# Kernel optimization log

Hardware: AMD Instinct MI355X
Metric: run time of the kernel (lower is better)

Reference implementation:

```python
import jax, jax.numpy as jnp
import numpy as np

EMBED_DIM = 1024
NUM_HEADS = 16
HEAD_DIM = EMBED_DIM // NUM_HEADS


def setup_inputs() -> dict:
    key = jax.random.key(0)
    ks = jax.random.split(key, 9)
    B, S, D = 2, 2048, EMBED_DIM
    scale = 1.0 / np.sqrt(D)
    x = jax.random.normal(ks[0], (B, S, D), dtype=jnp.float32)
    # Linear params (torch nn.Linear: y = x @ W.T + b); store W as [out, in]
    Wq = jax.random.normal(ks[1], (D, D), dtype=jnp.float32) * scale
    bq = jnp.zeros((D,), dtype=jnp.float32)
    Wk = jax.random.normal(ks[2], (D, D), dtype=jnp.float32) * scale
    bk = jnp.zeros((D,), dtype=jnp.float32)
    Wv = jax.random.normal(ks[3], (D, D), dtype=jnp.float32) * scale
    bv = jnp.zeros((D,), dtype=jnp.float32)
    Wo = jax.random.normal(ks[4], (D, D), dtype=jnp.float32) * scale
    bo = jnp.zeros((D,), dtype=jnp.float32)
    return {"x": x, "Wq": Wq, "bq": bq, "Wk": Wk, "bk": bk,
            "Wv": Wv, "bv": bv, "Wo": Wo, "bo": bo}


def reference(x, Wq, bq, Wk, bk, Wv, bv, Wo, bo):
    B, S, D = x.shape
    H, Hd = NUM_HEADS, HEAD_DIM
    scaling = Hd ** -0.5
    # projections (torch Linear: x @ W.T + b)
    q = (x @ Wq.T + bq).reshape(B, S, H, Hd).transpose(0, 2, 1, 3)  # [B,H,S,Hd]
    k = (x @ Wk.T + bk).reshape(B, S, H, Hd).transpose(0, 2, 1, 3)
    v = (x @ Wv.T + bv).reshape(B, S, H, Hd).transpose(0, 2, 1, 3)
    # full score matrix, as in the original (no flash tiling)
    scores = jnp.einsum('bhqd,bhkd->bhqk', q, k) * scaling  # [B,H,S,S]
    attn = jax.nn.softmax(scores, axis=-1)
    # dropout is identity in eval mode
    out = jnp.einsum('bhqk,bhkd->bhqd', attn, v)  # [B,H,S,Hd]
    out = out.transpose(0, 2, 1, 3).reshape(B, S, D)
    return out @ Wo.T + bo
```

## Files before the change

### kernel.cpp

```cpp
#include <hip/hip_runtime.h>
#include <stdint.h>

typedef unsigned short u16;
typedef short short8 __attribute__((ext_vector_type(8)));
typedef float f32x4 __attribute__((ext_vector_type(4)));
typedef float f32x16 __attribute__((ext_vector_type(16)));
typedef float f32x2 __attribute__((ext_vector_type(2)));

__device__ __forceinline__ u16 f2bf_fast(float f) {
  union { float f; uint32_t u; } x;
  x.f = f;
  return (u16)((x.u + 0x8000u) >> 16);
}

__device__ __forceinline__ uint32_t pack2bf(float lo, float hi) {
  union { float f; uint32_t u; } a, b;
  a.f = lo; b.f = hi;
  return __builtin_amdgcn_perm(b.u + 0x8000u, a.u + 0x8000u, 0x07060302u);
}

__device__ __forceinline__ float bf2f(uint32_t u) {
  union { uint32_t u; float f; } x;
  x.u = u << 16;
  return x.f;
}

__device__ __forceinline__ uint32_t cvtpk(float lo, float hi) {
  uint32_t r;
  asm("v_cvt_pk_bf16_f32 %0, %1, %2" : "=v"(r) : "v"(lo), "v"(hi));
  return r;
}

__device__ __forceinline__ void permswap(uint32_t& a, uint32_t& b) {
  asm("v_permlane32_swap_b32 %0, %1" : "+v"(a), "+v"(b));
}

__device__ __forceinline__ void gload_lds16(const void* g, void* l) {
  __builtin_amdgcn_global_load_lds(
      (const __attribute__((address_space(1))) void*)g,
      (__attribute__((address_space(3))) void*)l, 16, 0, 0);
}

__device__ __forceinline__ f32x4 mfma16(short8 a, short8 b, f32x4 c) {
  return __builtin_amdgcn_mfma_f32_16x16x32_bf16(a, b, c, 0, 0, 0);
}

__device__ __forceinline__ f32x16 mfma32(short8 a, short8 b, f32x16 c) {
  return __builtin_amdgcn_mfma_f32_32x32x16_bf16(a, b, c, 0, 0, 0);
}

#define QSCALE 0.18033688011112042f

__global__ void pack_all(const float* __restrict__ x, const float* __restrict__ wq,
                         const float* __restrict__ wk, const float* __restrict__ wv,
                         const float* __restrict__ wo, u16* __restrict__ xp,
                         u16* __restrict__ wp) {
  const int gi = blockIdx.x * 256 + threadIdx.x;
  const int lane = gi & 63;
  const int kc = (gi >> 6) & 31;
  const int rt = gi >> 11;
  const int col = kc * 32 + (lane >> 4) * 8;
  const float* src;
  int row;
  if (rt < 256) {
    src = x;
    row = rt * 16 + (lane & 15);
  } else {
    const int wti = rt - 256;
    const int widx = wti >> 6;
    src = (widx == 0) ? wq : (widx == 1) ? wk : (widx == 2) ? wv : wo;
    row = (wti & 63) * 16 + (lane & 15);
  }
  const float4* p = (const float4*)(src + (size_t)row * 1024 + col);
  const float4 v0 = p[0], v1 = p[1];
  uint4 o;
  o.x = pack2bf(v0.x, v0.y);
  o.y = pack2bf(v0.z, v0.w);
  o.z = pack2bf(v1.x, v1.y);
  o.w = pack2bf(v1.z, v1.w);
  u16* dst = (rt < 256) ? xp : wp;
  const int og = (rt < 256) ? gi : gi - 524288;
  ((uint4*)dst)[og] = o;
}

__global__ __launch_bounds__(256, 3) void proj_qkv(
    const u16* __restrict__ xp, const u16* __restrict__ wp,
    const float* __restrict__ bq, const float* __restrict__ bk,
    const float* __restrict__ bv, u16* __restrict__ qw, u16* __restrict__ kw,
    u16* __restrict__ vw) {
  __shared__ __align__(16) u16 As[8192];
  __shared__ __align__(16) u16 Bs[8192];
  const int tid = threadIdx.x, lane = tid & 63, w = tid >> 6;
  const int quad = lane >> 4, l15 = lane & 15;

  const int bid = blockIdx.x;
  const int work = (bid & 7) * 96 + (bid >> 3);
  const bool isQK = work < 512;
  int at0, bt0, bm2, bn2;
  const u16 *Ap, *Bp;
  if (isQK) {
    bm2 = work >> 4; bn2 = work & 15;
    Ap = xp; at0 = bm2 * 8;
    Bp = wp; bt0 = bn2 * 8;
  } else {
    const int h = work - 512;
    bm2 = h >> 5; bn2 = h & 31;
    Ap = wp; at0 = 128 + bm2 * 8;
    Bp = xp; bt0 = bn2 * 8;
  }
  const int wr = w >> 1, wc = w & 1;
  const int bm = bm2 * 2 + wr, bn = bn2 * 2 + wc;

  auto stage = [&](int kc, int buf) {
#pragma unroll
    for (int i = 0; i < 4; ++i) {
      const int g = w * 4 + i;
      const int t = g & 7;
      const u16* src = (g < 8)
          ? (Ap + (((at0 + t) << 5) + kc) * 512 + lane * 8)
          : (Bp + (((bt0 + t) << 5) + kc) * 512 + lane * 8);
      u16* dst = ((g < 8) ? As : Bs) + (buf * 8 + t) * 512 + lane * 8;
      gload_lds16(src, dst);
    }
  };

  f32x4 acc[4][4] = {};

  stage(0, 0);
  __syncthreads();

  for (int kc = 0; kc < 32; ++kc) {
    const int cur = kc & 1;
    if (kc < 31) stage(kc + 1, cur ^ 1);

    const u16* Ab = As + cur * 4096;
    const u16* Bb = Bs + cur * 4096;
    short8 af[4], bf[4];
#pragma unroll
    for (int mt = 0; mt < 4; ++mt)
      af[mt] = *(const short8*)&Ab[((wr * 4 + mt) * 64 + lane) * 8];
#pragma unroll
    for (int nt = 0; nt < 4; ++nt)
      bf[nt] = *(const short8*)&Bb[((wc * 4 + nt) * 64 + lane) * 8];

#pragma unroll
    for (int mt = 0; mt < 4; ++mt)
#pragma unroll
      for (int nt = 0; nt < 4; ++nt)
        acc[mt][nt] = mfma16(af[mt], bf[nt], acc[mt][nt]);
    __syncthreads();
  }

#pragma unroll
  for (int nt = 0; nt < 4; ++nt) {
    const int n = bn * 64 + nt * 16 + l15;
#pragma unroll
    for (int mt = 0; mt < 4; ++mt)
#pragma unroll
      for (int r = 0; r < 4; ++r) {
        const int m = bm * 64 + mt * 16 + quad * 4 + r;
        const float a = acc[mt][nt][r];
        if (isQK) {
          const bool isQ = (bn < 16);
          const int nn = isQ ? n : n - 1024;
          const float v = isQ ? (a + bq[nn]) * QSCALE : a + bk[nn];
          u16* op = isQ ? qw : kw;
          const int b = m >> 11, s = m & 2047, hh = nn >> 6, d = nn & 63;
          op[((size_t)((b * 16 + hh) * 2048 + s)) * 64 + d] = f2bf_fast(v);
        } else {
          const float v = a + bv[m];
          const int b = n >> 11, s = n & 2047;
          vw[((size_t)(b * 1024 + m)) * 2048 + s] = f2bf_fast(v);
        }
      }
  }
}

__global__ __launch_bounds__(512, 4) void attn_kernel(
    const u16* __restrict__ Q, const u16* __restrict__ Kt,
    const u16* __restrict__ Vt, u16* __restrict__ awp) {
  __shared__ __align__(16) u16 Sm[40960];
  const int tid = threadIdx.x, lane = tid & 63, w = tid >> 6;
  const int l31 = lane & 31, hi = lane >> 5, l7 = lane & 7;
  const int kh = w >> 2, qg = w & 3;
  const int qt = blockIdx.x;
  const int bh = blockIdx.y;

  const char* Qb = (const char*)(Q + ((size_t)bh * 2048 + qt * 128) * 64);
  const char* Kb = (const char*)(Kt + (size_t)bh * 2048 * 64);
  const char* Vb = (const char*)(Vt + (size_t)bh * 64 * 2048);

  auto stageKV = [&](int j, int buf) {
#pragma unroll
    for (int h = 0; h < 2; ++h) {
      const int kt = h * 16 + j;
      u16* Kl = Sm + (buf * 2 + h) * 8192;
      u16* Vl = Kl + 4096;
      const int G = w * 64 + lane;
      const int r = G >> 3, sl = G & 7;
      gload_lds16(Kb + (size_t)(kt * 64 + r) * 128 + ((sl ^ (r & 7)) * 16),
                  &Kl[G * 8]);
      gload_lds16(Vb + (size_t)r * 4096 + kt * 128 + ((sl ^ (r & 7)) * 16),
                  &Vl[G * 8]);
    }
  };

  u16* Qs = Sm + 32768;
#pragma unroll
  for (int i = 0; i < 2; ++i) {
    const int G = (w * 2 + i) * 64 + lane;
    const int row = G >> 3, sl = G & 7;
    gload_lds16(Qb + (size_t)row * 128 + ((sl ^ (row & 7)) * 16), &Qs[G * 8]);
  }
  stageKV(0, 0);
  __syncthreads();

  short8 aq[4];
#pragma unroll
  for (int ds = 0; ds < 4; ++ds)
    aq[ds] = *(const short8*)&Qs[(qg * 32 + l31) * 64 + (((ds << 1) + hi) ^ l7) * 8];

  f32x16 ot[2] = {};
  f32x2 l2 = {0.f, 0.f};

  for (int j = 0; j < 16; ++j) {
    const int buf = j & 1;
    if (j < 15) stageKV(j + 1, buf ^ 1);
    const u16* Kl = Sm + (buf * 2 + kh) * 8192;
    const u16* Vl = Kl + 4096;

#pragma unroll
    for (int t = 0; t < 2; ++t) {
      f32x16 st = {};
      __builtin_amdgcn_s_setprio(1);
#pragma unroll
      for (int ds = 0; ds < 4; ++ds) {
        short8 kf = *(const short8*)&Kl[(t * 32 + l31) * 64 +
                                        (((ds << 1) + hi) ^ l7) * 8];
        st = mfma32(kf, aq[ds], st);
      }
      __builtin_amdgcn_s_setprio(0);
      float e[16];
#pragma unroll
      for (int i = 0; i < 16; ++i) e[i] = __builtin_amdgcn_exp2f(st[i]);
#pragma unroll
      for (int i = 0; i < 8; ++i) l2 += (f32x2){e[2 * i], e[2 * i + 1]};

      uint32_t p01 = cvtpk(e[0], e[1]),   p23 = cvtpk(e[2], e[3]);
      uint32_t p45 = cvtpk(e[4], e[5]),   p67 = cvtpk(e[6], e[7]);
      uint32_t p89 = cvtpk(e[8], e[9]),   pAB = cvtpk(e[10], e[11]);
      uint32_t pCD = cvtpk(e[12], e[13]), pEF = cvtpk(e[14], e[15]);
      permswap(p01, p45);
      permswap(p23, p67);
      permswap(p89, pCD);
      permswap(pAB, pEF);
      union { uint32_t u[4]; short8 s; } b0, b1;
      b0.u[0] = p01; b0.u[1] = p23; b0.u[2] = p45; b0.u[3] = p67;
      b1.u[0] = p89; b1.u[1] = pAB; b1.u[2] = pCD; b1.u[3] = pEF;

      __builtin_amdgcn_s_setprio(1);
#pragma unroll
      for (int dt = 0; dt < 2; ++dt) {
#pragma unroll
        for (int s2 = 0; s2 < 2; ++s2) {
          short8 vf = *(const short8*)&Vl[(dt * 32 + l31) * 64 +
                                          ((((t * 2 + s2) << 1) + hi) ^ l7) * 8];
          ot[dt] = mfma32(vf, s2 ? b1.s : b0.s, ot[dt]);
        }
      }
      __builtin_amdgcn_s_setprio(0);
    }
    if (j < 15) __syncthreads();
  }

  float l = l2.x + l2.y;
  l += __shfl_xor(l, 32);

  __syncthreads();
  float* fb = (float*)Sm;
  if (kh == 1) {
    float* p = fb + (qg * 64 + lane) * 34;
#pragma unroll
    for (int i = 0; i < 8; ++i) {
      *(f32x2*)(p + 2 * i)      = (f32x2){ot[0][2 * i], ot[0][2 * i + 1]};
      *(f32x2*)(p + 16 + 2 * i) = (f32x2){ot[1][2 * i], ot[1][2 * i + 1]};
    }
    p[32] = l;
  }
  __syncthreads();
  if (kh == 0) {
    const float* p = fb + (qg * 64 + lane) * 34;
#pragma unroll
    for (int i = 0; i < 16; ++i) ot[0][i] += p[i];
#pragma unroll
    for (int i = 0; i < 16; ++i) ot[1][i] += p[16 + i];
    l += p[32];
    const float inv = __builtin_amdgcn_rcpf(l);

    const int b = bh >> 4, h = bh & 15;
    const int rt = b * 128 + qt * 8 + qg * 2 + (l31 >> 4);
#pragma unroll
    for (int dt = 0; dt < 2; ++dt) {
      const int kc = h * 2 + dt;
#pragma unroll
      for (int g = 0; g < 4; ++g) {
        const int ln = (lane & 15) + 16 * g;
        uint2 ov;
        ov.x = cvtpk(ot[dt][4 * g + 0] * inv, ot[dt][4 * g + 1] * inv);
        ov.y = cvtpk(ot[dt][4 * g + 2] * inv, ot[dt][4 * g + 3] * inv);
        *(uint2*)(awp + ((size_t)((rt * 32 + kc) * 64 + ln)) * 8 + hi * 4) = ov;
      }
    }
  }
}

__global__ __launch_bounds__(512, 2) void out_proj(const u16* __restrict__ awp,
                                                   const u16* __restrict__ wp,
                                                   const float* __restrict__ bo,
                                                   float* __restrict__ out) {
  __shared__ __align__(16) u16 As[8192];
  __shared__ __align__(16) u16 Bs[8192];
  const int tid = threadIdx.x, lane = tid & 63, w = tid >> 6;
  const int quad = lane >> 4, l15 = lane & 15;

  const int bid = blockIdx.x;
  const int work = (bid & 7) * 32 + (bid >> 3);
  const int bm2 = work >> 3, bn2 = work & 7;
  const int at0 = bm2 * 8, bt0 = 192 + bn2 * 8;
  const int wr = w >> 2, wc = w & 3;

  auto stage = [&](int kc, int buf) {
#pragma unroll
    for (int i = 0; i < 2; ++i) {
      const int g = w * 2 + i;
      const int t = g & 7;
      const u16* src = (g < 8)
          ? (awp + (((at0 + t) << 5) + kc) * 512 + lane * 8)
          : (wp + (((bt0 + t) << 5) + kc) * 512 + lane * 8);
      u16* dst = ((g < 8) ? As : Bs) + (buf * 8 + t) * 512 + lane * 8;
      gload_lds16(src, dst);
    }
  };

  f32x4 acc[4][2] = {};

  stage(0, 0);
  __syncthreads();

  for (int kc = 0; kc < 32; ++kc) {
    const int cur = kc & 1;
    if (kc < 31) stage(kc + 1, cur ^ 1);

    const u16* Ab = As + cur * 4096;
    const u16* Bb = Bs + cur * 4096;
    short8 af[4], bf[2];
#pragma unroll
    for (int mt = 0; mt < 4; ++mt)
      af[mt] = *(const short8*)&Ab[((wr * 4 + mt) * 64 + lane) * 8];
#pragma unroll
    for (int nt = 0; nt < 2; ++nt)
      bf[nt] = *(const short8*)&Bb[((wc * 2 + nt) * 64 + lane) * 8];

#pragma unroll
    for (int mt = 0; mt < 4; ++mt)
#pragma unroll
      for (int nt = 0; nt < 2; ++nt)
        acc[mt][nt] = mfma16(af[mt], bf[nt], acc[mt][nt]);
    __syncthreads();
  }

#pragma unroll
  for (int nt = 0; nt < 2; ++nt) {
    const int n = bn2 * 128 + wc * 32 + nt * 16 + l15;
    const float bb = bo[n];
#pragma unroll
    for (int mt = 0; mt < 4; ++mt)
#pragma unroll
      for (int r = 0; r < 4; ++r) {
        const int m = bm2 * 128 + wr * 64 + mt * 16 + quad * 4 + r;
        out[(size_t)m * 1024 + n] = acc[mt][nt][r] + bb;
      }
  }
}

extern "C" void kernel_launch(void* const* d_in, const int* in_sizes, int n_in,
                              void* d_out, int out_size, void* d_ws, size_t ws_size,
                              hipStream_t stream) {
  const float* x  = (const float*)d_in[0];
  const float* Wq = (const float*)d_in[1];
  const float* bq = (const float*)d_in[2];
  const float* Wk = (const float*)d_in[3];
  const float* bk = (const float*)d_in[4];
  const float* Wv = (const float*)d_in[5];
  const float* bv = (const float*)d_in[6];
  const float* Wo = (const float*)d_in[7];
  const float* bo = (const float*)d_in[8];

  const size_t M4 = (size_t)4 * 1024 * 1024;
  u16* xp  = (u16*)d_ws;
  u16* wp  = xp + M4;
  u16* qw  = wp + M4;
  u16* kw  = qw + M4;
  u16* vw  = kw + M4;
  u16* awp = vw + M4;

  pack_all<<<4096, 256, 0, stream>>>(x, Wq, Wk, Wv, Wo, xp, wp);

  proj_qkv<<<768, 256, 0, stream>>>(xp, wp, bq, bk, bv, qw, kw, vw);

  attn_kernel<<<dim3(16, 32), 512, 0, stream>>>(qw, kw, vw, awp);

  out_proj<<<256, 512, 0, stream>>>(awp, wp, bo, (float*)d_out);
}
```

Before: 189.3 us.

## Triple-buffer GEMM LDS staging with single barrier and batch attention MFMA phases

```diff
diff --git a/kernel.cpp b/kernel.cpp
--- a/kernel.cpp
+++ b/kernel.cpp
@@ -88,8 +88,8 @@
     const float* __restrict__ bq, const float* __restrict__ bk,
     const float* __restrict__ bv, u16* __restrict__ qw, u16* __restrict__ kw,
     u16* __restrict__ vw) {
-  __shared__ __align__(16) u16 As[8192];
-  __shared__ __align__(16) u16 Bs[8192];
+  __shared__ __align__(16) u16 As[12288];
+  __shared__ __align__(16) u16 Bs[12288];
   const int tid = threadIdx.x, lane = tid & 63, w = tid >> 6;
   const int quad = lane >> 4, l15 = lane & 15;
 
@@ -127,14 +127,19 @@
   f32x4 acc[4][4] = {};
 
   stage(0, 0);
-  __syncthreads();
-
+  stage(1, 1);
+
+#pragma unroll
   for (int kc = 0; kc < 32; ++kc) {
-    const int cur = kc & 1;
-    if (kc < 31) stage(kc + 1, cur ^ 1);
-
-    const u16* Ab = As + cur * 4096;
-    const u16* Bb = Bs + cur * 4096;
+    if (kc < 31)
+      asm volatile("s_waitcnt vmcnt(4)" ::: "memory");
+    else
+      asm volatile("s_waitcnt vmcnt(0)" ::: "memory");
+    __builtin_amdgcn_s_barrier();
+    if (kc < 30) stage(kc + 2, (kc + 2) % 3);
+
+    const u16* Ab = As + (kc % 3) * 4096;
+    const u16* Bb = Bs + (kc % 3) * 4096;
     short8 af[4], bf[4];
 #pragma unroll
     for (int mt = 0; mt < 4; ++mt)
@@ -148,7 +153,6 @@
 #pragma unroll
       for (int nt = 0; nt < 4; ++nt)
         acc[mt][nt] = mfma16(af[mt], bf[nt], acc[mt][nt]);
-    __syncthreads();
   }
 
 #pragma unroll
@@ -229,23 +233,29 @@
     const u16* Kl = Sm + (buf * 2 + kh) * 8192;
     const u16* Vl = Kl + 4096;
 
+    f32x16 st[2];
+    __builtin_amdgcn_s_setprio(1);
 #pragma unroll
     for (int t = 0; t < 2; ++t) {
-      f32x16 st = {};
-      __builtin_amdgcn_s_setprio(1);
+      f32x16 s = {};
 #pragma unroll
       for (int ds = 0; ds < 4; ++ds) {
         short8 kf = *(const short8*)&Kl[(t * 32 + l31) * 64 +
                                         (((ds << 1) + hi) ^ l7) * 8];
-        st = mfma32(kf, aq[ds], st);
+        s = mfma32(kf, aq[ds], s);
       }
-      __builtin_amdgcn_s_setprio(0);
+      st[t] = s;
+    }
+    __builtin_amdgcn_s_setprio(0);
+
+    union { uint32_t u[4]; short8 s; } pb[2][2];
+#pragma unroll
+    for (int t = 0; t < 2; ++t) {
       float e[16];
 #pragma unroll
-      for (int i = 0; i < 16; ++i) e[i] = __builtin_amdgcn_exp2f(st[i]);
+      for (int i = 0; i < 16; ++i) e[i] = __builtin_amdgcn_exp2f(st[t][i]);
 #pragma unroll
       for (int i = 0; i < 8; ++i) l2 += (f32x2){e[2 * i], e[2 * i + 1]};
-
       uint32_t p01 = cvtpk(e[0], e[1]),   p23 = cvtpk(e[2], e[3]);
       uint32_t p45 = cvtpk(e[4], e[5]),   p67 = cvtpk(e[6], e[7]);
       uint32_t p89 = cvtpk(e[8], e[9]),   pAB = cvtpk(e[10], e[11]);
@@ -254,22 +264,23 @@
       permswap(p23, p67);
       permswap(p89, pCD);
       permswap(pAB, pEF);
-      union { uint32_t u[4]; short8 s; } b0, b1;
-      b0.u[0] = p01; b0.u[1] = p23; b0.u[2] = p45; b0.u[3] = p67;
-      b1.u[0] = p89; b1.u[1] = pAB; b1.u[2] = pCD; b1.u[3] = pEF;
-
-      __builtin_amdgcn_s_setprio(1);
-#pragma unroll
-      for (int dt = 0; dt < 2; ++dt) {
+      pb[t][0].u[0] = p01; pb[t][0].u[1] = p23; pb[t][0].u[2] = p45; pb[t][0].u[3] = p67;
+      pb[t][1].u[0] = p89; pb[t][1].u[1] = pAB; pb[t][1].u[2] = pCD; pb[t][1].u[3] = pEF;
+    }
+
+    __builtin_amdgcn_s_setprio(1);
+#pragma unroll
+    for (int t = 0; t < 2; ++t)
+#pragma unroll
+      for (int dt = 0; dt < 2; ++dt)
 #pragma unroll
         for (int s2 = 0; s2 < 2; ++s2) {
           short8 vf = *(const short8*)&Vl[(dt * 32 + l31) * 64 +
                                           ((((t * 2 + s2) << 1) + hi) ^ l7) * 8];
-          ot[dt] = mfma32(vf, s2 ? b1.s : b0.s, ot[dt]);
+          ot[dt] = mfma32(vf, pb[t][s2].s, ot[dt]);
         }
-      }
-      __builtin_amdgcn_s_setprio(0);
-    }
+    __builtin_amdgcn_s_setprio(0);
+
     if (j < 15) __syncthreads();
   }
 
@@ -318,8 +329,8 @@
                                                    const u16* __restrict__ wp,
                                                    const float* __restrict__ bo,
                                                    float* __restrict__ out) {
-  __shared__ __align__(16) u16 As[8192];
-  __shared__ __align__(16) u16 Bs[8192];
+  __shared__ __align__(16) u16 As[12288];
+  __shared__ __align__(16) u16 Bs[12288];
   const int tid = threadIdx.x, lane = tid & 63, w = tid >> 6;
   const int quad = lane >> 4, l15 = lane & 15;
 
@@ -345,14 +356,19 @@
   f32x4 acc[4][2] = {};
 
   stage(0, 0);
-  __syncthreads();
-
+  stage(1, 1);
+
+#pragma unroll
   for (int kc = 0; kc < 32; ++kc) {
-    const int cur = kc & 1;
-    if (kc < 31) stage(kc + 1, cur ^ 1);
-
-    const u16* Ab = As + cur * 4096;
-    const u16* Bb = Bs + cur * 4096;
+    if (kc < 31)
+      asm volatile("s_waitcnt vmcnt(2)" ::: "memory");
+    else
+      asm volatile("s_waitcnt vmcnt(0)" ::: "memory");
+    __builtin_amdgcn_s_barrier();
+    if (kc < 30) stage(kc + 2, (kc + 2) % 3);
+
+    const u16* Ab = As + (kc % 3) * 4096;
+    const u16* Bb = Bs + (kc % 3) * 4096;
     short8 af[4], bf[2];
 #pragma unroll
     for (int mt = 0; mt < 4; ++mt)
@@ -366,7 +382,6 @@
 #pragma unroll
       for (int nt = 0; nt < 2; ++nt)
         acc[mt][nt] = mfma16(af[mt], bf[nt], acc[mt][nt]);
-    __syncthreads();
   }
 
 #pragma unroll
```

Result: faster. 181.8 us (-3.9%).
